# Kernel tuning notes

Hardware: AMD Instinct MI355X
Metric: run time of the kernel (lower is better)

## Reference

```python
import jax, jax.numpy as jnp
import numpy as np
import math

B, S, D, H, PD = 2, 2048, 1024, 16, 3
DK = D // H          # 64
SP = S // H          # 128, required so physics_scores matches scores shape


def setup_inputs() -> dict:
    key = jax.random.key(0)
    ks = jax.random.split(key, 16)
    sc = 0.02
    return {
        "query": jax.random.normal(ks[0], (B, S, D), jnp.float32),
        "key_in": jax.random.normal(ks[1], (B, S, D), jnp.float32),
        "value": jax.random.normal(ks[2], (B, S, D), jnp.float32),
        "physics_info": jax.random.normal(ks[3], (B, SP, PD), jnp.float32),
        "Wq": jax.random.normal(ks[4], (D, D), jnp.float32) * sc,
        "bq": jnp.zeros((D,), jnp.float32),
        "Wk": jax.random.normal(ks[5], (D, D), jnp.float32) * sc,
        "bk": jnp.zeros((D,), jnp.float32),
        "Wv": jax.random.normal(ks[6], (D, D), jnp.float32) * sc,
        "bv": jnp.zeros((D,), jnp.float32),
        "Wo": jax.random.normal(ks[7], (D, D), jnp.float32) * sc,
        "bo": jnp.zeros((D,), jnp.float32),
        "Pw": jax.random.normal(ks[8], (PD, D), jnp.float32),   # physics_weight
        "pb": jnp.zeros((1,), jnp.float32),                      # physics_bias
    }


def reference(query, key_in, value, physics_info, Wq, bq, Wk, bk, Wv, bv, Wo, bo, Pw, pb):
    b, s, d = query.shape
    inv = 1.0 / math.sqrt(DK)
    # project and split heads -> [B, H, S, DK]
    Q = (query @ Wq + bq).reshape(b, s, H, DK).transpose(0, 2, 1, 3)
    K = (key_in @ Wk + bk).reshape(b, s, H, DK).transpose(0, 2, 1, 3)
    V = (value @ Wv + bv).reshape(b, s, H, DK).transpose(0, 2, 1, 3)
    scores = jnp.einsum('bhqd,bhkd->bhqk', Q, K) * inv  # [B,H,S,S]
    # physics constraint: [B,SP,D] -> (expand over heads is a no-op) -> [B,SP*H,DK]
    pc = (physics_info @ Pw).reshape(b, SP * H, DK)
    physics_scores = jnp.einsum('bhqd,bkd->bhqk', Q, pc) * inv  # [B,H,S,S]
    scores = scores + pb[0] * physics_scores
    attn = jax.nn.softmax(scores, axis=-1)  # dropout in eval mode (identity)
    ctx = jnp.einsum('bhqk,bhkd->bhqd', attn, V)
    ctx = ctx.transpose(0, 2, 1, 3).reshape(b, s, d)
    return ctx @ Wo + bo
```

## Files before the change

### kernel.cpp

```cpp
#include <hip/hip_runtime.h>
#include <hip/hip_bf16.h>
#include <stdint.h>
#include <math.h>

typedef __bf16 bf16_t;
typedef __attribute__((ext_vector_type(8))) __bf16 bf16x8;
typedef __attribute__((ext_vector_type(4))) __bf16 bf16x4;
typedef __attribute__((ext_vector_type(4))) short short4_t;
typedef __attribute__((ext_vector_type(4))) float f32x4;

#define GLOBAL_AS(p) ((const __attribute__((address_space(1))) void*)(p))
#define LDS_AS(p)    ((__attribute__((address_space(3))) void*)(p))

#define B_ 2
#define S_ 2048
#define D_ 1024
#define H_ 16
#define DK_ 64
#define SP_ 128

#define QSCALE 0.1803368801111144f

static __device__ inline float fast_exp2(float x) {
#if __has_builtin(__builtin_amdgcn_exp2f)
    return __builtin_amdgcn_exp2f(x);
#else
    return __expf(x * 0.6931471805599453f);
#endif
}

static __device__ inline f32x4 mfma16x16x16bf16(short4_t a, short4_t b, f32x4 c) {
#if __has_builtin(__builtin_amdgcn_mfma_f32_16x16x16bf16_1k)
    return __builtin_amdgcn_mfma_f32_16x16x16bf16_1k(a, b, c, 0, 0, 0);
#else
    asm volatile("v_mfma_f32_16x16x16_bf16 %0, %1, %2, %0" : "+v"(c) : "v"(a), "v"(b));
    return c;
#endif
}

struct WPtrs { const float* w[4]; bf16_t* o[4]; };

__global__ __launch_bounds__(256) void prep(
    const float* __restrict__ q, const float* __restrict__ k,
    const float* __restrict__ v,
    bf16_t* __restrict__ qo, bf16_t* __restrict__ ko, bf16_t* __restrict__ vo,
    WPtrs wp, const float* __restrict__ phys, const float* __restrict__ Pw,
    float* __restrict__ PP) {
    int bx = blockIdx.x, tid = threadIdx.x;
    if (bx < 6144) {
        int z = bx >> 11, blk = bx & 2047;
        const float* in = (z == 0) ? q : (z == 1) ? k : v;
        bf16_t* out = (z == 0) ? qo : (z == 1) ? ko : vo;
        size_t i = ((size_t)blk * 256 + tid) * 8;
        f32x4 a = *(const f32x4*)(in + i);
        f32x4 b = *(const f32x4*)(in + i + 4);
        bf16x8 o;
#pragma unroll
        for (int e = 0; e < 4; ++e) { o[e] = (bf16_t)a[e]; o[4 + e] = (bf16_t)b[e]; }
        *(bf16x8*)(out + i) = o;
    } else if (bx < 10240) {
        __shared__ bf16_t t[32][33];
        int idx = bx - 6144;
        int z = idx >> 10;
        const float* W = wp.w[z];
        bf16_t* Wt = wp.o[z];
        int gx = (idx & 31) * 32, gy = ((idx >> 5) & 31) * 32;
        int x = tid & 31, y0 = tid >> 5;
#pragma unroll
        for (int j = 0; j < 32; j += 8)
            t[y0 + j][x] = (bf16_t)W[(size_t)(gy + y0 + j) * D_ + gx + x];
        __syncthreads();
#pragma unroll
        for (int j = 0; j < 32; j += 8)
            Wt[(size_t)(gx + y0 + j) * D_ + gy + x] = t[x][y0 + j];
    } else {
        int i = (bx - 10240) * 256 + tid;
        int n = i & (D_ - 1);
        int sb = i >> 10;
        float acc = 0.f;
#pragma unroll
        for (int p = 0; p < 3; ++p)
            acc += phys[sb * 3 + p] * Pw[p * D_ + n];
        PP[i] = acc;
    }
}

#define TSTR 272

__global__ __launch_bounds__(256) void qkv_gemm(
    const bf16_t* __restrict__ Qi, const bf16_t* __restrict__ Ki,
    const bf16_t* __restrict__ Vi,
    const bf16_t* __restrict__ WqT, const bf16_t* __restrict__ WkT,
    const bf16_t* __restrict__ WvT,
    const float* __restrict__ bq, const float* __restrict__ bk,
    const float* __restrict__ bv,
    bf16_t* __restrict__ Qo, bf16_t* __restrict__ Ko, bf16_t* __restrict__ Vo,
    const float* __restrict__ PP, const float* __restrict__ pbp) {
    __shared__ alignas(16) char smem[40960];
    bf16_t* lA = (bf16_t*)smem;
    bf16_t* lB = (bf16_t*)(smem + 16384);
    int z = blockIdx.z;
    const bf16_t* A = (z == 0) ? Qi : (z == 1) ? Ki : Vi;
    const bf16_t* Bt = (z == 0) ? WqT : (z == 1) ? WkT : WvT;
    const float* bias = (z == 0) ? bq : (z == 1) ? bk : bv;

    int tid = threadIdx.x;
    int lane = tid & 63, wid = tid >> 6;
    int quad = lane >> 4, l15 = lane & 15;
    int bm = blockIdx.x * 128;
    int bn = blockIdx.y * 128;
    int wm = (wid >> 1) * 64, wn = (wid & 1) * 64;
    f32x4 acc[4][4] = {};

    for (int k0 = 0; k0 < D_; k0 += 64) {
        __syncthreads();
        const char* gA = (const char*)(A + (size_t)bm * D_ + k0);
        const char* gB = (const char*)(Bt + (size_t)bn * D_ + k0);
#pragma unroll
        for (int j = 0; j < 4; ++j) {
            int woff = j * 4096 + wid * 1024;
            int fl = woff + lane * 16;
            int row = fl >> 7, col = fl & 127;
            __builtin_amdgcn_global_load_lds(GLOBAL_AS(gA + (size_t)row * (D_ * 2) + col),
                                             LDS_AS((char*)lA + woff), 16, 0, 0);
            __builtin_amdgcn_global_load_lds(GLOBAL_AS(gB + (size_t)row * (D_ * 2) + col),
                                             LDS_AS((char*)lB + woff), 16, 0, 0);
        }
        __syncthreads();
#pragma unroll
        for (int ks = 0; ks < 2; ++ks) {
            bf16x8 af[4], bfr[4];
#pragma unroll
            for (int i = 0; i < 4; ++i) {
                af[i] = *(const bf16x8*)((const char*)lA + (wm + i * 16 + l15) * 128 + ks * 64 + quad * 16);
                bfr[i] = *(const bf16x8*)((const char*)lB + (wn + i * 16 + l15) * 128 + ks * 64 + quad * 16);
            }
#pragma unroll
            for (int i = 0; i < 4; ++i)
#pragma unroll
                for (int j = 0; j < 4; ++j)
                    acc[i][j] = __builtin_amdgcn_mfma_f32_16x16x32_bf16(af[i], bfr[j], acc[i][j], 0, 0, 0);
        }
    }

    __syncthreads();
    float pb0 = (z == 1) ? pbp[0] : 0.f;
    char* T = smem;
#pragma unroll
    for (int i = 0; i < 4; ++i)
#pragma unroll
        for (int j = 0; j < 4; ++j) {
            int rl0 = wm + i * 16 + quad * 4;
            int c = wn + j * 16 + l15;
            float bv_ = bias[bn + c];
            if (z == 2) {
                bf16x4 t4;
#pragma unroll
                for (int reg = 0; reg < 4; ++reg) t4[reg] = (bf16_t)(acc[i][j][reg] + bv_);
                *(bf16x4*)(T + c * TSTR + rl0 * 2) = t4;
            } else if (z == 1) {
#pragma unroll
                for (int reg = 0; reg < 4; ++reg) {
                    int r = bm + rl0 + reg;
                    int b = r >> 11, s = r & (S_ - 1);
                    float v = acc[i][j][reg] + bv_ +
                              pb0 * PP[((size_t)(b * SP_ + (s >> 4)) << 10) + ((s & 15) << 6) + ((bn + c) & 63)];
                    *(bf16_t*)(T + (rl0 + reg) * TSTR + c * 2) = (bf16_t)v;
                }
            } else {
#pragma unroll
                for (int reg = 0; reg < 4; ++reg)
                    *(bf16_t*)(T + (rl0 + reg) * TSTR + c * 2) = (bf16_t)((acc[i][j][reg] + bv_) * QSCALE);
            }
        }
    __syncthreads();
    if (z == 2) {
        int b = bm >> 11, s0 = bm & (S_ - 1);
        char* gout = (char*)Vo + (((size_t)(b << 10) + bn) * S_ + s0) * 2;
#pragma unroll
        for (int it = 0; it < 8; ++it) {
            int chunk = it * 256 + tid;
            int row = chunk >> 4, c16 = chunk & 15;
            bf16x8 v = *(const bf16x8*)(T + row * TSTR + c16 * 16);
            *(bf16x8*)(gout + (size_t)row * (S_ * 2) + c16 * 16) = v;
        }
    } else {
        bf16_t* O = (z == 0) ? Qo : Ko;
        char* gout = (char*)(O + (size_t)bm * D_ + bn);
#pragma unroll
        for (int it = 0; it < 8; ++it) {
            int chunk = it * 256 + tid;
            int row = chunk >> 4, c16 = chunk & 15;
            bf16x8 v = *(const bf16x8*)(T + row * TSTR + c16 * 16);
            *(bf16x8*)(gout + (size_t)row * (D_ * 2) + c16 * 16) = v;
        }
    }
}

#define KSTR 144
#define VSTR 272

__global__ __launch_bounds__(256) void flash_attn(const bf16_t* Qb,
                                                  const bf16_t* __restrict__ Kb,
                                                  const bf16_t* __restrict__ Vt,
                                                  bf16_t* Ctx) {
    __shared__ alignas(16) char lK[128 * KSTR];
    __shared__ alignas(16) char lV[64 * VSTR];
    int tid = threadIdx.x, lane = tid & 63, wid = tid >> 6;
    int quad = lane >> 4, l15 = lane & 15;
    int q0 = blockIdx.x * 128;
    int h = blockIdx.y, b = blockIdx.z;
    const bf16_t* Qh = Qb + ((size_t)b * S_) * D_ + h * DK_;
    const bf16_t* Kh = Kb + ((size_t)b * S_) * D_ + h * DK_;
    const bf16_t* Vh = Vt + ((size_t)b * D_ + h * DK_) * S_;

    {
        const char* g = (const char*)(Qh + (size_t)q0 * D_);
#pragma unroll
        for (int j = 0; j < 4; ++j) {
            int flat = j * 4096 + tid * 16;
            bf16x8 v = *(const bf16x8*)(g + (size_t)(flat >> 7) * (D_ * 2) + (flat & 127));
            *(bf16x8*)(lK + (flat >> 7) * KSTR + (flat & 127)) = v;
        }
    }
    __syncthreads();
    bf16x8 qf[2][2];
#pragma unroll
    for (int mt = 0; mt < 2; ++mt)
#pragma unroll
        for (int ks = 0; ks < 2; ++ks)
            qf[mt][ks] = *(const bf16x8*)(lK + (wid * 32 + mt * 16 + l15) * KSTR + ks * 64 + quad * 16);

    f32x4 ot[4][2] = {};
    float l_i[2] = {0.f, 0.f};

    for (int t = 0; t < S_ / 128; ++t) {
        const char* gK = (const char*)(Kh + (size_t)t * 128 * D_);
        const char* gV = (const char*)(Vh + (size_t)t * 128);
        bf16x8 vk[4], vv[4];
#pragma unroll
        for (int j = 0; j < 4; ++j) {
            int flat = j * 4096 + tid * 16;
            vk[j] = *(const bf16x8*)(gK + (size_t)(flat >> 7) * (D_ * 2) + (flat & 127));
            vv[j] = *(const bf16x8*)(gV + (size_t)(flat >> 8) * (S_ * 2) + (flat & 255));
        }
        __syncthreads();
#pragma unroll
        for (int j = 0; j < 4; ++j) {
            int flat = j * 4096 + tid * 16;
            *(bf16x8*)(lK + (flat >> 7) * KSTR + (flat & 127)) = vk[j];
            *(bf16x8*)(lV + (flat >> 8) * VSTR + (flat & 255)) = vv[j];
        }
        __syncthreads();

        f32x4 sc[8][2];
#pragma unroll
        for (int kt = 0; kt < 8; ++kt)
#pragma unroll
            for (int mt = 0; mt < 2; ++mt) sc[kt][mt] = (f32x4){0.f, 0.f, 0.f, 0.f};
#pragma unroll
        for (int kt = 0; kt < 8; ++kt) {
            bf16x8 kf0 = *(const bf16x8*)(lK + (kt * 16 + l15) * KSTR + quad * 16);
            bf16x8 kf1 = *(const bf16x8*)(lK + (kt * 16 + l15) * KSTR + 64 + quad * 16);
#pragma unroll
            for (int mt = 0; mt < 2; ++mt) {
                sc[kt][mt] = __builtin_amdgcn_mfma_f32_16x16x32_bf16(kf0, qf[mt][0], sc[kt][mt], 0, 0, 0);
                sc[kt][mt] = __builtin_amdgcn_mfma_f32_16x16x32_bf16(kf1, qf[mt][1], sc[kt][mt], 0, 0, 0);
            }
        }

#pragma unroll
        for (int mt = 0; mt < 2; ++mt) {
            float rsum = 0.f;
#pragma unroll
            for (int kt = 0; kt < 8; ++kt)
#pragma unroll
                for (int r = 0; r < 4; ++r) {
                    float p = fast_exp2(sc[kt][mt][r]);
                    sc[kt][mt][r] = p;
                    rsum += p;
                }
            rsum += __shfl_xor(rsum, 16, 64);
            rsum += __shfl_xor(rsum, 32, 64);
            l_i[mt] += rsum;
        }

#pragma unroll
        for (int kt = 0; kt < 8; ++kt) {
            short4_t bp[2];
#pragma unroll
            for (int mt = 0; mt < 2; ++mt) {
                bf16x4 t4;
#pragma unroll
                for (int r = 0; r < 4; ++r) t4[r] = (bf16_t)sc[kt][mt][r];
                bp[mt] = *(short4_t*)&t4;
            }
#pragma unroll
            for (int dt = 0; dt < 4; ++dt) {
                bf16x4 a4 = *(const bf16x4*)(lV + (dt * 16 + l15) * VSTR + kt * 32 + quad * 8);
                short4_t ap = *(short4_t*)&a4;
#pragma unroll
                for (int mt = 0; mt < 2; ++mt)
                    ot[dt][mt] = mfma16x16x16bf16(ap, bp[mt], ot[dt][mt]);
            }
        }
    }

    __syncthreads();
#pragma unroll
    for (int mt = 0; mt < 2; ++mt) {
        float inv_l = 1.0f / l_i[mt];
#pragma unroll
        for (int dt = 0; dt < 4; ++dt) {
            bf16x4 t4;
#pragma unroll
            for (int r = 0; r < 4; ++r) t4[r] = (bf16_t)(ot[dt][mt][r] * inv_l);
            *(bf16x4*)(lK + (wid * 32 + mt * 16 + l15) * KSTR + dt * 32 + quad * 8) = t4;
        }
    }
    __syncthreads();
    {
        char* gout = (char*)(Ctx + ((size_t)b * S_ + q0) * D_ + h * DK_);
#pragma unroll
        for (int j = 0; j < 4; ++j) {
            int flat = j * 4096 + tid * 16;
            bf16x8 v = *(const bf16x8*)(lK + (flat >> 7) * KSTR + (flat & 127));
            *(bf16x8*)(gout + (size_t)(flat >> 7) * (D_ * 2) + (flat & 127)) = v;
        }
    }
}

__global__ __launch_bounds__(256) void gemm_out(const bf16_t* __restrict__ A,
                                                const bf16_t* __restrict__ Bt,
                                                const float* __restrict__ bias,
                                                float* __restrict__ C) {
    __shared__ alignas(16) bf16_t lA[128 * 64];
    __shared__ alignas(16) bf16_t lB[128 * 64];
    int tid = threadIdx.x;
    int lane = tid & 63, wid = tid >> 6;
    int quad = lane >> 4, l15 = lane & 15;
    int bm = blockIdx.x * 128;
    int bn = blockIdx.y * 128;
    int wm = (wid >> 1) * 64, wn = (wid & 1) * 64;
    f32x4 acc[4][4] = {};

    for (int k0 = 0; k0 < D_; k0 += 64) {
        __syncthreads();
        const char* gA = (const char*)(A + (size_t)bm * D_ + k0);
        const char* gB = (const char*)(Bt + (size_t)bn * D_ + k0);
#pragma unroll
        for (int j = 0; j < 4; ++j) {
            int woff = j * 4096 + wid * 1024;
            int fl = woff + lane * 16;
            int row = fl >> 7, col = fl & 127;
            __builtin_amdgcn_global_load_lds(GLOBAL_AS(gA + (size_t)row * (D_ * 2) + col),
                                             LDS_AS((char*)lA + woff), 16, 0, 0);
            __builtin_amdgcn_global_load_lds(GLOBAL_AS(gB + (size_t)row * (D_ * 2) + col),
                                             LDS_AS((char*)lB + woff), 16, 0, 0);
        }
        __syncthreads();
#pragma unroll
        for (int ks = 0; ks < 2; ++ks) {
            bf16x8 af[4], bfr[4];
#pragma unroll
            for (int i = 0; i < 4; ++i) {
                af[i] = *(const bf16x8*)((const char*)lA + (wm + i * 16 + l15) * 128 + ks * 64 + quad * 16);
                bfr[i] = *(const bf16x8*)((const char*)lB + (wn + i * 16 + l15) * 128 + ks * 64 + quad * 16);
            }
#pragma unroll
            for (int i = 0; i < 4; ++i)
#pragma unroll
                for (int j = 0; j < 4; ++j)
                    acc[i][j] = __builtin_amdgcn_mfma_f32_16x16x32_bf16(af[i], bfr[j], acc[i][j], 0, 0, 0);
        }
    }
#pragma unroll
    for (int i = 0; i < 4; ++i)
#pragma unroll
        for (int j = 0; j < 4; ++j) {
            int r0 = bm + wm + i * 16 + quad * 4;
            int c = bn + wn + j * 16 + l15;
            float bv_ = bias[c];
#pragma unroll
            for (int reg = 0; reg < 4; ++reg)
                C[(size_t)(r0 + reg) * D_ + c] = acc[i][j][reg] + bv_;
        }
}

extern "C" void kernel_launch(void* const* d_in, const int* in_sizes, int n_in,
                              void* d_out, int out_size, void* d_ws, size_t ws_size,
                              hipStream_t stream) {
    const float* query  = (const float*)d_in[0];
    const float* key_in = (const float*)d_in[1];
    const float* value  = (const float*)d_in[2];
    const float* phys   = (const float*)d_in[3];
    const float* Wq     = (const float*)d_in[4];
    const float* bq     = (const float*)d_in[5];
    const float* Wk     = (const float*)d_in[6];
    const float* bk     = (const float*)d_in[7];
    const float* Wv     = (const float*)d_in[8];
    const float* bv     = (const float*)d_in[9];
    const float* Wo     = (const float*)d_in[10];
    const float* bo     = (const float*)d_in[11];
    const float* Pw     = (const float*)d_in[12];
    const float* pb     = (const float*)d_in[13];

    char* ws = (char*)d_ws;
    const size_t MB = 1ull << 20;
    bf16_t* Kb  = (bf16_t*)(ws + 0 * MB);
    bf16_t* QC  = (bf16_t*)(ws + 8 * MB);
    bf16_t* Kin = (bf16_t*)(ws + 16 * MB);
    bf16_t* Vin = (bf16_t*)(ws + 24 * MB);
    bf16_t* WqT = (bf16_t*)(ws + 32 * MB);
    bf16_t* WkT = (bf16_t*)(ws + 34 * MB);
    bf16_t* WvT = (bf16_t*)(ws + 36 * MB);
    bf16_t* WoT = (bf16_t*)(ws + 38 * MB);
    float*  PP  = (float*)(ws + 40 * MB);
    bf16_t* Vt  = (bf16_t*)d_out;
    bf16_t* Qin = (bf16_t*)((char*)d_out + 8 * MB);

    WPtrs wp;
    wp.w[0] = Wq; wp.w[1] = Wk; wp.w[2] = Wv; wp.w[3] = Wo;
    wp.o[0] = WqT; wp.o[1] = WkT; wp.o[2] = WvT; wp.o[3] = WoT;

    prep<<<11264, 256, 0, stream>>>(query, key_in, value, Qin, Kin, Vin,
                                    wp, phys, Pw, PP);

    dim3 gq(32, 8, 3);
    qkv_gemm<<<gq, 256, 0, stream>>>(Qin, Kin, Vin, WqT, WkT, WvT,
                                     bq, bk, bv, QC, Kb, Vt, PP, pb);

    dim3 fg(S_ / 128, H_, B_);
    flash_attn<<<fg, 256, 0, stream>>>(QC, Kb, Vt, QC);

    dim3 gg(32, 8);
    gemm_out<<<gg, 256, 0, stream>>>(QC, WoT, bo, (float*)d_out);
}
```

Before: 249.2 us.

## Use 16x16x32 MFMA for PV with bpermute-repacked P and packed bf16 converts

The P·V product switches from the 16x16x16 bf16 MFMA to the 16x16x32 instruction, halving the number of MFMA issues. The probability fragments are converted with packed v_cvt_pk_bf16_f32 and redistributed across lanes with ds_bpermute to match the wider K operand layout, and V is read in 8-element vectors. s_setprio is raised around both MFMA loops to favour matrix issue. The added cross-lane permutes cost LDS crossbar traffic and some select instructions.

Result: no change. 253.2 us (+1.6%).

```diff
diff --git a/kernel.cpp b/kernel.cpp
--- a/kernel.cpp
+++ b/kernel.cpp
@@ -8,6 +8,7 @@
 typedef __attribute__((ext_vector_type(4))) __bf16 bf16x4;
 typedef __attribute__((ext_vector_type(4))) short short4_t;
 typedef __attribute__((ext_vector_type(4))) float f32x4;
+typedef __attribute__((ext_vector_type(4))) unsigned int u32x4;
 
 #define GLOBAL_AS(p) ((const __attribute__((address_space(1))) void*)(p))
 #define LDS_AS(p)    ((__attribute__((address_space(3))) void*)(p))
@@ -26,15 +27,6 @@
     return __builtin_amdgcn_exp2f(x);
 #else
     return __expf(x * 0.6931471805599453f);
-#endif
-}
-
-static __device__ inline f32x4 mfma16x16x16bf16(short4_t a, short4_t b, f32x4 c) {
-#if __has_builtin(__builtin_amdgcn_mfma_f32_16x16x16bf16_1k)
-    return __builtin_amdgcn_mfma_f32_16x16x16bf16_1k(a, b, c, 0, 0, 0);
-#else
-    asm volatile("v_mfma_f32_16x16x16_bf16 %0, %1, %2, %0" : "+v"(c) : "v"(a), "v"(b));
-    return c;
 #endif
 }
 
@@ -258,6 +250,7 @@
         for (int kt = 0; kt < 8; ++kt)
 #pragma unroll
             for (int mt = 0; mt < 2; ++mt) sc[kt][mt] = (f32x4){0.f, 0.f, 0.f, 0.f};
+        __builtin_amdgcn_s_setprio(1);
 #pragma unroll
         for (int kt = 0; kt < 8; ++kt) {
             bf16x8 kf0 = *(const bf16x8*)(lK + (kt * 16 + l15) * KSTR + quad * 16);
@@ -268,6 +261,7 @@
                 sc[kt][mt] = __builtin_amdgcn_mfma_f32_16x16x32_bf16(kf1, qf[mt][1], sc[kt][mt], 0, 0, 0);
             }
         }
+        __builtin_amdgcn_s_setprio(0);
 
 #pragma unroll
         for (int mt = 0; mt < 2; ++mt) {
@@ -285,25 +279,48 @@
             l_i[mt] += rsum;
         }
 
-#pragma unroll
-        for (int kt = 0; kt < 8; ++kt) {
-            short4_t bp[2];
+        __builtin_amdgcn_s_setprio(1);
+#pragma unroll
+        for (int c = 0; c < 4; ++c) {
+            u32x4 bpv[2];
 #pragma unroll
             for (int mt = 0; mt < 2; ++mt) {
-                bf16x4 t4;
-#pragma unroll
-                for (int r = 0; r < 4; ++r) t4[r] = (bf16_t)sc[kt][mt][r];
-                bp[mt] = *(short4_t*)&t4;
+                unsigned int w0a, w1a, w0b, w1b;
+                asm("v_cvt_pk_bf16_f32 %0, %1, %2"
+                    : "=v"(w0a) : "v"(sc[2 * c][mt][0]), "v"(sc[2 * c][mt][1]));
+                asm("v_cvt_pk_bf16_f32 %0, %1, %2"
+                    : "=v"(w1a) : "v"(sc[2 * c][mt][2]), "v"(sc[2 * c][mt][3]));
+                asm("v_cvt_pk_bf16_f32 %0, %1, %2"
+                    : "=v"(w0b) : "v"(sc[2 * c + 1][mt][0]), "v"(sc[2 * c + 1][mt][1]));
+                asm("v_cvt_pk_bf16_f32 %0, %1, %2"
+                    : "=v"(w1b) : "v"(sc[2 * c + 1][mt][2]), "v"(sc[2 * c + 1][mt][3]));
+                int idxA = (((quad & 1) << 5) + l15) << 2;
+                int idxB = idxA + 64;
+                int a0 = __builtin_amdgcn_ds_bpermute(idxA, (int)w0a);
+                int a1 = __builtin_amdgcn_ds_bpermute(idxA, (int)w1a);
+                int a2 = __builtin_amdgcn_ds_bpermute(idxB, (int)w0a);
+                int a3 = __builtin_amdgcn_ds_bpermute(idxB, (int)w1a);
+                int b0 = __builtin_amdgcn_ds_bpermute(idxA, (int)w0b);
+                int b1 = __builtin_amdgcn_ds_bpermute(idxA, (int)w1b);
+                int b2 = __builtin_amdgcn_ds_bpermute(idxB, (int)w0b);
+                int b3 = __builtin_amdgcn_ds_bpermute(idxB, (int)w1b);
+                bool hi = quad >= 2;
+                bpv[mt][0] = (unsigned int)(hi ? b0 : a0);
+                bpv[mt][1] = (unsigned int)(hi ? b1 : a1);
+                bpv[mt][2] = (unsigned int)(hi ? b2 : a2);
+                bpv[mt][3] = (unsigned int)(hi ? b3 : a3);
             }
 #pragma unroll
             for (int dt = 0; dt < 4; ++dt) {
-                bf16x4 a4 = *(const bf16x4*)(lV + (dt * 16 + l15) * VSTR + kt * 32 + quad * 8);
-                short4_t ap = *(short4_t*)&a4;
-#pragma unroll
-                for (int mt = 0; mt < 2; ++mt)
-                    ot[dt][mt] = mfma16x16x16bf16(ap, bp[mt], ot[dt][mt]);
-            }
-        }
+                bf16x8 ap = *(const bf16x8*)(lV + (dt * 16 + l15) * VSTR + c * 64 + quad * 16);
+#pragma unroll
+                for (int mt = 0; mt < 2; ++mt) {
+                    bf16x8 bp8 = *(bf16x8*)&bpv[mt];
+                    ot[dt][mt] = __builtin_amdgcn_mfma_f32_16x16x32_bf16(ap, bp8, ot[dt][mt], 0, 0, 0);
+                }
+            }
+        }
+        __builtin_amdgcn_s_setprio(0);
     }
 
     __syncthreads();
```
